# Kernel optimization log

Hardware: AMD Instinct MI355X
Metric: run time of the kernel (lower is better)

Reference implementation:

```python
import jax, jax.numpy as jnp
import numpy as np

B, S, D, V = 4, 1024, 512, 8192
SCALES = [1, 2, 4, 8, 16]   # nn.Parameter init; used via int(scale.item()) -> static
WIN = 8                     # min(8, S//2) in compute_semantic_coherence
EPS = 1e-5


def layer_norm(x, g, b):
    m = x.mean(-1, keepdims=True)
    v = ((x - m) ** 2).mean(-1, keepdims=True)
    return (x - m) / jnp.sqrt(v + EPS) * g + b


def setup_inputs() -> dict:
    key = jax.random.key(0)
    ks = jax.random.split(key, 24)
    n = lambda k, shape, s=0.02: (jax.random.normal(k, shape, jnp.float32) * s)
    return {
        "embeddings": jax.random.normal(ks[0], (B, S, D), jnp.float32),
        "token_ids": jax.random.randint(ks[1], (B, S), 0, V),
        "context_mask": jnp.ones((B, S), jnp.float32),
        "token_similarity": n(ks[2], (V, V)),
        "W_scale": n(ks[3], (len(SCALES), D), 0.05), "b_scale": jnp.zeros((D,), jnp.float32),
        "W_sem": n(ks[4], (1, D), 0.05), "b_sem": jnp.zeros((D,), jnp.float32),
        "W_ctx": n(ks[5], (D, D), 0.02), "b_ctx": jnp.zeros((D,), jnp.float32),
        "W_fuse": n(ks[6], (4 * D, D), 0.02), "b_fuse": jnp.zeros((D,), jnp.float32),
        "ln1_g": jnp.ones((D,), jnp.float32), "ln1_b": jnp.zeros((D,), jnp.float32),
        "ln2_g": jnp.ones((D,), jnp.float32), "ln2_b": jnp.zeros((D,), jnp.float32),
        "ln3_g": jnp.ones((D,), jnp.float32), "ln3_b": jnp.zeros((D,), jnp.float32),
        "W_e0": n(ks[7], (D, D), 0.02), "b_e0": jnp.zeros((D,), jnp.float32),
        "W_e1": n(ks[8], (D, D), 0.02), "b_e1": jnp.zeros((D,), jnp.float32),
        "W_e2": n(ks[9], (D, D), 0.02), "b_e2": jnp.zeros((D,), jnp.float32),
    }


def _forward(embeddings, token_ids, context_mask, token_similarity,
             W_scale, b_scale, W_sem, b_sem, W_ctx, b_ctx, W_fuse, b_fuse,
             ln1_g, ln1_b, ln2_g, ln2_b, ln3_g, ln3_b,
             W_e0, b_e0, W_e1, b_e1, W_e2, b_e2):
    phases = jnp.tanh(embeddings)  # [B,S,D]

    # --- multi-scale coherence via cumulative sums + cos angle-difference identity ---
    # mean_t cos(p_t - m) = cos(m)*mean(cos p) + sin(m)*mean(sin p) over each window
    z = jnp.zeros((B, 1, D), phases.dtype)
    cum_p = jnp.concatenate([z, jnp.cumsum(phases, 1)], 1)            # [B,S+1,D]
    cum_c = jnp.concatenate([z, jnp.cumsum(jnp.cos(phases), 1)], 1)
    cum_s = jnp.concatenate([z, jnp.cumsum(jnp.sin(phases), 1)], 1)
    cols = []
    for s in SCALES:
        wm = (cum_p[:, s:] - cum_p[:, :-s]) / s   # window mean  [B,S-s+1,D]
        ac = (cum_c[:, s:] - cum_c[:, :-s]) / s   # window mean cos
        asn = (cum_s[:, s:] - cum_s[:, :-s]) / s  # window mean sin
        coh = jnp.mean(jnp.cos(wm) * ac + jnp.sin(wm) * asn, -1)      # [B,S-s+1]
        cols.append(jnp.pad(coh, ((0, 0), (0, s - 1))))               # torch leaves tail zeros
    msc = jnp.stack(cols, -1)                                         # [B,S,num_scales]
    scale_coh = msc @ W_scale + b_scale                               # [B,S,D]

    # --- semantic coherence (windowed, sim-weighted; torch takes mean over WHOLE tensor incl. batch) ---
    te = token_similarity[token_ids]                                  # [B,S,V]
    ten = te / jnp.maximum(jnp.linalg.norm(te, axis=-1, keepdims=True), 1e-12)
    tsim = jnp.einsum('biv,bjv->bij', ten, ten)                       # [B,S,S]
    off = jnp.arange(-WIN, WIN + 1)
    pos = jnp.arange(S)[:, None] + off[None, :]                       # [S,17]
    valid = (pos >= 0) & (pos < S)
    posc = jnp.clip(pos, 0, S - 1)
    pwin = phases[:, posc]                                            # [B,S,17,D]
    swin = jnp.take_along_axis(tsim, jnp.broadcast_to(posc[None], (B, S, 2 * WIN + 1)), axis=2)
    coh = jnp.cos((phases[:, :, None, :] - pwin) * swin[..., None]) * valid[None, :, :, None].astype(phases.dtype)
    counts = valid.sum(1).astype(phases.dtype)                        # [S]
    sem = coh.sum((0, 2, 3)) / (B * counts * D)                       # [S] (same scalar for all batches)
    sem = jnp.broadcast_to(sem[None, :], (B, S))[..., None]           # [B,S,1]
    sem_coh = sem @ W_sem + b_sem                                     # [B,S,D]

    # --- context coherence (context_mask path) ---
    cmean = jnp.mean(embeddings * context_mask[..., None], 1, keepdims=True)
    ctx_coh = jnp.cos(embeddings - cmean) @ W_ctx + b_ctx

    # --- local coherence ---
    lc = jnp.cos(embeddings[:, 1:] - embeddings[:, :-1])
    lc = jnp.concatenate([lc, jnp.zeros((B, 1, D), embeddings.dtype)], 1)

    allc = jnp.concatenate([scale_coh, sem_coh, ctx_coh, lc], -1)     # [B,S,4D]
    x = layer_norm(allc @ W_fuse + b_fuse, ln1_g, ln1_b)
    x = jax.nn.gelu(x, approximate=False)                             # dropout = identity (eval)
    for W, bb in ((W_e0, b_e0), (W_e1, b_e1), (W_e2, b_e2)):
        r = x
        h = layer_norm(x, ln2_g, ln2_b) @ W + bb
        x = r + jax.nn.gelu(h, approximate=False) * 0.1
    return layer_norm(x, ln3_g, ln3_b)


def reference(embeddings, token_ids, context_mask, token_similarity,
              W_scale, b_scale, W_sem, b_sem, W_ctx, b_ctx, W_fuse, b_fuse,
              ln1_g, ln1_b, ln2_g, ln2_b, ln3_g, ln3_b,
              W_e0, b_e0, W_e1, b_e1, W_e2, b_e2):
    return _forward(embeddings, token_ids, context_mask, token_similarity,
                    W_scale, b_scale, W_sem, b_sem, W_ctx, b_ctx, W_fuse, b_fuse,
                    ln1_g, ln1_b, ln2_g, ln2_b, ln3_g, ln3_b,
                    W_e0, b_e0, W_e1, b_e1, W_e2, b_e2)
```

## Files before the change

kernel.cpp:

```cpp
#include <hip/hip_runtime.h>


#define DEV __device__ __forceinline__
typedef unsigned short u16;
typedef __bf16 bf16x8 __attribute__((ext_vector_type(8)));
typedef float f32x4 __attribute__((ext_vector_type(4)));

static constexpr int S = 1024;
static constexpr int D = 512;
static constexpr int KCAT = 1056;

DEV u16 f2bf(float f) {
  unsigned u = __float_as_uint(f);
  return (u16)((u + 0x7fffu + ((u >> 16) & 1u)) >> 16);
}
DEV float gelu(float x) { return 0.5f * x * (1.f + erff(x * 0.70710678118654752f)); }
DEV float wred(float v) {
#pragma unroll
  for (int off = 32; off; off >>= 1) v += __shfl_down(v, off, 64);
  return v;
}
DEV void bred2(float& a, float& b, float* sm, int tid) {
  a = wred(a); b = wred(b);
  int w = tid >> 6;
  if ((tid & 63) == 0) { sm[w] = a; sm[w + 4] = b; }
  __syncthreads();
  a = sm[0] + sm[1] + sm[2] + sm[3];
  b = sm[4] + sm[5] + sm[6] + sm[7];
  __syncthreads();
}

__global__ __launch_bounds__(256) void k_pre(const float* __restrict__ emb,
                                             const float* __restrict__ mask,
                                             float* __restrict__ ph,
                                             float* __restrict__ cmacc) {
  int blk = blockIdx.x, tid = threadIdx.x;
  if (blk < 1024) {
    int idx = blk * 256 + tid;
#pragma unroll
    for (int r = 0; r < 2; ++r, idx += 262144) {
      float4 v = ((const float4*)emb)[idx];
      float4 o;
      o.x = tanhf(v.x); o.y = tanhf(v.y); o.z = tanhf(v.z); o.w = tanhf(v.w);
      ((float4*)ph)[idx] = o;
    }
  } else {
    int r = blk - 1024, b = r >> 3, chunk = r & 7;
    float a0 = 0.f, a1 = 0.f;
    for (int s = chunk * 128; s < chunk * 128 + 128; ++s) {
      float m = mask[b * S + s];
      const float* row = emb + (size_t)(b * S + s) * D;
      a0 += row[tid] * m; a1 += row[tid + 256] * m;
    }
    atomicAdd(cmacc + b * D + tid, a0);
    atomicAdd(cmacc + b * D + tid + 256, a1);
  }
}

static constexpr int DP = 77;
__global__ __launch_bounds__(256) void k_dots(const float* __restrict__ sim,
                                              const int* __restrict__ tok,
                                              float* __restrict__ dots_raw,
                                              float* __restrict__ normsq) {
  __shared__ float sT[256 * DP];
  __shared__ int stok[72];
  int bx = blockIdx.x, cy = blockIdx.y, tid = threadIdx.x;
  int b = bx >> 4, g0 = (bx & 15) * 64;
  int gidx = b * S + g0;
  if (tid < 72) {
    int p = g0 + tid;
    stok[tid] = (p < S) ? tok[b * S + p] : -1;
  }
  __syncthreads();
  int c = tid, cbase = cy * 256;
#pragma unroll 3
  for (int it = 0; it < 18; ++it) {
#pragma unroll
    for (int j = 0; j < 4; ++j) {
      int tk = stok[it * 4 + j];
      sT[c * DP + it * 4 + j] = (tk >= 0) ? sim[(size_t)tk * 8192 + cbase + c] : 0.f;
    }
  }
  __syncthreads();
  int wave = tid >> 6, lane = tid & 63;
  float acc[9] = {};
#pragma unroll 2
  for (int cc = 0; cc < 64; ++cc) {
    const float* row = &sT[(wave * 64 + cc) * DP];
    float va = row[lane];
    acc[8] += va * va;
#pragma unroll
    for (int o = 1; o <= 8; ++o) acc[o - 1] += va * row[lane + o];
  }
  __syncthreads();
  float* red = sT;
#pragma unroll
  for (int s = 0; s < 9; ++s) red[(wave * 9 + s) * 64 + lane] = acc[s];
  __syncthreads();
  for (int u = tid; u < 576; u += 256) {
    int s = u >> 6, a = u & 63;
    float v = red[s * 64 + a] + red[(9 + s) * 64 + a] +
              red[(18 + s) * 64 + a] + red[(27 + s) * 64 + a];
    if (s < 8) atomicAdd(&dots_raw[(size_t)(gidx + a) * 8 + s], v);
    else       atomicAdd(&normsq[gidx + a], v);
  }
}

__global__ __launch_bounds__(256) void k_coh(const float* __restrict__ ph,
                                             const float* __restrict__ dots_raw,
                                             const float* __restrict__ normsq,
                                             float* __restrict__ msc,
                                             float* __restrict__ semacc) {
  __shared__ float sw[4][17];
  int wave = threadIdx.x >> 6, lane = threadIdx.x & 63;
  int idx = blockIdx.x * 4 + wave, i = idx & 1023;
  if (lane < 17) {
    int o = lane - 8, j = i + o;
    float v = 0.f;
    if (j >= 0 && j < S) {
      if (o == 0) v = 1.f;
      else {
        float dr = (o > 0) ? dots_raw[(size_t)idx * 8 + o - 1]
                           : dots_raw[(size_t)(idx + o) * 8 + (-o - 1)];
        float ni = fmaxf(sqrtf(normsq[idx]), 1e-12f);
        float nj = fmaxf(sqrtf(normsq[idx + o]), 1e-12f);
        v = dr / (ni * nj);
      }
    }
    sw[wave][lane] = v;
  }
  __syncthreads();
  int jmax = (S - 1 - i < 15) ? (S - 1 - i) : 15;
  float a0 = 0.f, a1 = 0.f, a2 = 0.f, a3 = 0.f, a4 = 0.f, asem = 0.f;
  for (int it = 0; it < 8; ++it) {
    int d = lane + it * 64;
    float p[24];
#pragma unroll
    for (int t = 0; t < 24; ++t) {
      int o = t - 8, j = i + o;
      int oc = (j >= 0 && j < S) ? o : 0;
      p[t] = ph[(size_t)(idx + oc) * D + d];
    }
    float sp = 0.f, sc = 0.f, ss = 0.f;
#pragma unroll
    for (int j = 0; j < 16; ++j) {
      float x = (j <= jmax) ? p[j + 8] : 0.f;
      sp += x; sc += __cosf(x); ss += __sinf(x);
      if (j == 0) a0 += __cosf(sp) * sc + __sinf(sp) * ss;
      else if (j == 1)  { float wm = sp * 0.5f;    a1 += __cosf(wm) * (sc * 0.5f)    + __sinf(wm) * (ss * 0.5f); }
      else if (j == 3)  { float wm = sp * 0.25f;   a2 += __cosf(wm) * (sc * 0.25f)   + __sinf(wm) * (ss * 0.25f); }
      else if (j == 7)  { float wm = sp * 0.125f;  a3 += __cosf(wm) * (sc * 0.125f)  + __sinf(wm) * (ss * 0.125f); }
      else if (j == 15) { float wm = sp * 0.0625f; a4 += __cosf(wm) * (sc * 0.0625f) + __sinf(wm) * (ss * 0.0625f); }
    }
    float p0 = p[8];
#pragma unroll
    for (int oi = 0; oi < 17; ++oi) {
      int o = oi - 8, j = i + o;
      bool valid = (j >= 0) && (j < S);
      float sv = sw[wave][oi];
      asem += valid ? __cosf((p0 - p[oi]) * sv) : 0.f;
    }
  }
  a0 = wred(a0); a1 = wred(a1); a2 = wred(a2); a3 = wred(a3); a4 = wred(a4);
  asem = wred(asem);
  if (lane == 0) {
    float* o = msc + (size_t)idx * 5;
    o[0] = a0 * (1.f / 512.f);
    o[1] = (jmax >= 1)  ? a1 * (1.f / 512.f) : 0.f;
    o[2] = (jmax >= 3)  ? a2 * (1.f / 512.f) : 0.f;
    o[3] = (jmax >= 7)  ? a3 * (1.f / 512.f) : 0.f;
    o[4] = (jmax >= 15) ? a4 * (1.f / 512.f) : 0.f;
    atomicAdd(semacc + i, asem);
  }
}

__global__ __launch_bounds__(256) void k_wbig(const float* __restrict__ W0,
    const float* __restrict__ W1, const float* __restrict__ W2,
    const float* __restrict__ Wf, const float* __restrict__ wctx,
    const float* __restrict__ Wsc, const float* __restrict__ Wsm,
    const float* __restrict__ bsc, const float* __restrict__ bsm,
    const float* __restrict__ bcx,
    u16* __restrict__ T0, u16* __restrict__ T1, u16* __restrict__ T2,
    u16* __restrict__ wcatT, float* __restrict__ ctx_acc,
    float* __restrict__ sm_acc) {
  __shared__ float tile[64][65];
  int blk = blockIdx.x, tid = threadIdx.x;
  if (blk < 256) {
    int z = blk >> 6, rem = blk & 63;
    const float* src = z == 0 ? W0 : z == 1 ? W1 : z == 2 ? W2 : Wf + (size_t)1536 * 512;
    int r0 = (rem >> 3) * 64, c0 = (rem & 7) * 64;
    int tr = tid >> 6, tc = tid & 63;
#pragma unroll 4
    for (int i = 0; i < 16; ++i)
      tile[tr + i * 4][tc] = src[(size_t)(r0 + tr + i * 4) * 512 + c0 + tc];
    __syncthreads();
#pragma unroll 4
    for (int i = 0; i < 16; ++i) {
      int n = c0 + tr + i * 4, k = r0 + tc;
      u16 v = f2bf(tile[tc][tr + i * 4]);
      if (z == 3) wcatT[(size_t)n * KCAT + 512 + k] = v;
      else (z == 0 ? T0 : z == 1 ? T1 : T2)[(size_t)n * 512 + k] = v;
    }
  } else if (blk < 512) {
    int rem = blk - 256;
    int n = (rem & 1) * 256 + tid;
    int kbase = ((rem & 63) >> 1) * 16;
    int j0 = (rem >> 6) * 128;
    float acc[16] = {};
    for (int j = j0; j < j0 + 128; ++j) {
      float wf3 = Wf[(size_t)(1024 + j) * 512 + n];
#pragma unroll
      for (int kk = 0; kk < 16; ++kk) acc[kk] += wctx[(size_t)(kbase + kk) * 512 + j] * wf3;
    }
#pragma unroll
    for (int kk = 0; kk < 16; ++kk)
      atomicAdd(&ctx_acc[(size_t)(kbase + kk) * 512 + n], acc[kk]);
  } else {
    int rem = blk - 512;
    int n = (rem & 1) * 256 + tid;
    int j0 = (rem >> 1) * 16;
    float a0 = 0.f, a1 = 0.f, a2 = 0.f, a3 = 0.f, a4 = 0.f, au = 0.f, ac = 0.f;
    for (int j = j0; j < j0 + 16; ++j) {
      float wf1 = Wf[(size_t)j * 512 + n];
      float wf2 = Wf[(size_t)(512 + j) * 512 + n];
      float wf3 = Wf[(size_t)(1024 + j) * 512 + n];
      a0 += Wsc[j] * wf1; a1 += Wsc[512 + j] * wf1; a2 += Wsc[1024 + j] * wf1;
      a3 += Wsc[1536 + j] * wf1; a4 += Wsc[2048 + j] * wf1;
      au += Wsm[j] * wf2;
      ac += bsc[j] * wf1 + bsm[j] * wf2 + bcx[j] * wf3;
    }
    atomicAdd(&sm_acc[0 * 512 + n], a0);
    atomicAdd(&sm_acc[1 * 512 + n], a1);
    atomicAdd(&sm_acc[2 * 512 + n], a2);
    atomicAdd(&sm_acc[3 * 512 + n], a3);
    atomicAdd(&sm_acc[4 * 512 + n], a4);
    atomicAdd(&sm_acc[5 * 512 + n], au);
    atomicAdd(&sm_acc[6 * 512 + n], ac);
  }
}

__global__ __launch_bounds__(256) void k_packfin(const float* __restrict__ ctx_acc,
    const float* __restrict__ sm_acc, const float* __restrict__ bfu,
    u16* __restrict__ wcatT) {
  __shared__ float tile[64][65];
  int blk = blockIdx.x, tid = threadIdx.x;
  if (blk < 64) {
    int r0 = (blk >> 3) * 64, c0 = (blk & 7) * 64;
    int tr = tid >> 6, tc = tid & 63;
#pragma unroll 4
    for (int i = 0; i < 16; ++i)
      tile[tr + i * 4][tc] = ctx_acc[(size_t)(r0 + tr + i * 4) * 512 + c0 + tc];
    __syncthreads();
#pragma unroll 4
    for (int i = 0; i < 16; ++i)
      wcatT[(size_t)(c0 + tr + i * 4) * KCAT + r0 + tc] = f2bf(tile[tc][tr + i * 4]);
  } else {
    int n = (blk - 64) * 256 + tid;
    u16* row = wcatT + (size_t)n * KCAT;
#pragma unroll
    for (int s = 0; s < 6; ++s) row[1024 + s] = f2bf(sm_acc[s * 512 + n]);
    row[1030] = f2bf(sm_acc[6 * 512 + n] + bfu[n]);
    for (int k = 1031; k < KCAT; ++k) row[k] = 0;
  }
}

__global__ __launch_bounds__(256) void k_xcat(const float* __restrict__ emb,
    const float* __restrict__ cmacc, const float* __restrict__ msc,
    const float* __restrict__ semacc, u16* __restrict__ xcat) {
  int idx = blockIdx.x, b = idx >> 10, i = idx & 1023, tid = threadIdx.x;
  const float* erow = emb + (size_t)idx * D;
  u16* orow = xcat + (size_t)idx * KCAT;
  for (int c = tid; c < KCAT; c += 256) {
    float v;
    if (c < 512) {
      v = __cosf(erow[c] - cmacc[b * D + c] * (1.f / 1024.f));
    } else if (c < 1024) {
      int d = c - 512;
      v = (i < S - 1) ? __cosf(erow[D + d] - erow[d]) : 0.f;
    } else if (c < 1029) {
      v = msc[(size_t)idx * 5 + (c - 1024)];
    } else if (c == 1029) {
      int cnt = ((i < 8) ? i : 8) + ((S - 1 - i < 8) ? (S - 1 - i) : 8) + 1;
      v = semacc[i] / (4.f * (float)cnt * 512.f);
    } else if (c == 1030) {
      v = 1.f;
    } else v = 0.f;
    orow[c] = f2bf(v);
  }
}

__global__ __launch_bounds__(256) void k_gemm(const u16* __restrict__ A,
    const u16* __restrict__ BT, float* __restrict__ C,
    const float* __restrict__ bias, int K) {
  __shared__ __align__(16) u16 sA[64 * 40];
  __shared__ __align__(16) u16 sB[64 * 40];
  int tid = threadIdx.x, wave = tid >> 6, lane = tid & 63;
  int m0 = blockIdx.x * 64, n0 = blockIdx.y * 64;
  int lr = tid >> 2, lc = (tid & 3) * 8;
  int q8 = (lane >> 4) * 8, l15 = lane & 15;
  const u16* Ap = A + (size_t)(m0 + lr) * K + lc;
  const u16* Bp = BT + (size_t)(n0 + lr) * K + lc;
  f32x4 acc[4] = {};
  for (int k0 = 0; k0 < K; k0 += 32) {
    *(uint4*)&sA[lr * 40 + lc] = *(const uint4*)(Ap + k0);
    *(uint4*)&sB[lr * 40 + lc] = *(const uint4*)(Bp + k0);
    __syncthreads();
    bf16x8 af = *(const bf16x8*)&sA[(wave * 16 + l15) * 40 + q8];
#pragma unroll
    for (int f = 0; f < 4; ++f) {
      bf16x8 bfr = *(const bf16x8*)&sB[(f * 16 + l15) * 40 + q8];
      acc[f] = __builtin_amdgcn_mfma_f32_16x16x32_bf16(af, bfr, acc[f], 0, 0, 0);
    }
    __syncthreads();
  }
  int r0 = m0 + wave * 16 + (lane >> 4) * 4;
#pragma unroll
  for (int f = 0; f < 4; ++f) {
    int col = n0 + f * 16 + l15;
    float bv = bias ? bias[col] : 0.f;
#pragma unroll
    for (int r = 0; r < 4; ++r)
      C[(size_t)(r0 + r) * 512 + col] = acc[f][r] + bv;
  }
}

__global__ __launch_bounds__(256) void k_post_y1(const float* __restrict__ y,
    float* __restrict__ x, u16* __restrict__ t,
    const float* __restrict__ g1, const float* __restrict__ b1,
    const float* __restrict__ g2, const float* __restrict__ b2) {
  __shared__ float sm[8];
  int row = blockIdx.x, tid = threadIdx.x;
  size_t base = (size_t)row * 512;
  float v0 = y[base + tid], v1 = y[base + tid + 256];
  float s = v0 + v1, ss = v0 * v0 + v1 * v1;
  bred2(s, ss, sm, tid);
  float m = s * (1.f / 512.f);
  float inv = rsqrtf(ss * (1.f / 512.f) - m * m + 1e-5f);
  float x0 = gelu((v0 - m) * inv * g1[tid] + b1[tid]);
  float x1 = gelu((v1 - m) * inv * g1[tid + 256] + b1[tid + 256]);
  x[base + tid] = x0; x[base + tid + 256] = x1;
  s = x0 + x1; ss = x0 * x0 + x1 * x1;
  bred2(s, ss, sm, tid);
  m = s * (1.f / 512.f);
  inv = rsqrtf(ss * (1.f / 512.f) - m * m + 1e-5f);
  t[base + tid] = f2bf((x0 - m) * inv * g2[tid] + b2[tid]);
  t[base + tid + 256] = f2bf((x1 - m) * inv * g2[tid + 256] + b2[tid + 256]);
}

__global__ __launch_bounds__(256) void k_post_res(const float* __restrict__ h,
    float* __restrict__ x, u16* __restrict__ t, float* __restrict__ out,
    const float* __restrict__ g, const float* __restrict__ bb, int final_) {
  __shared__ float sm[8];
  int row = blockIdx.x, tid = threadIdx.x;
  size_t base = (size_t)row * 512;
  float x0 = x[base + tid] + 0.1f * gelu(h[base + tid]);
  float x1 = x[base + tid + 256] + 0.1f * gelu(h[base + tid + 256]);
  float s = x0 + x1, ss = x0 * x0 + x1 * x1;
  bred2(s, ss, sm, tid);
  float m = s * (1.f / 512.f);
  float inv = rsqrtf(ss * (1.f / 512.f) - m * m + 1e-5f);
  float n0 = (x0 - m) * inv * g[tid] + bb[tid];
  float n1 = (x1 - m) * inv * g[tid + 256] + bb[tid + 256];
  if (final_) {
    out[base + tid] = n0; out[base + tid + 256] = n1;
  } else {
    x[base + tid] = x0; x[base + tid + 256] = x1;
    t[base + tid] = f2bf(n0); t[base + tid + 256] = f2bf(n1);
  }
}

extern "C" void kernel_launch(void* const* d_in, const int* in_sizes, int n_in,
                              void* d_out, int out_size, void* d_ws, size_t ws_size,
                              hipStream_t stream) {
  const float* emb     = (const float*)d_in[0];
  const int*   tok     = (const int*)d_in[1];
  const float* mask    = (const float*)d_in[2];
  const float* sim     = (const float*)d_in[3];
  const float* W_scale = (const float*)d_in[4];
  const float* b_scale = (const float*)d_in[5];
  const float* W_sem   = (const float*)d_in[6];
  const float* b_sem   = (const float*)d_in[7];
  const float* W_ctx   = (const float*)d_in[8];
  const float* b_ctx   = (const float*)d_in[9];
  const float* W_fuse  = (const float*)d_in[10];
  const float* b_fuse  = (const float*)d_in[11];
  const float* ln1_g = (const float*)d_in[12], *ln1_b = (const float*)d_in[13];
  const float* ln2_g = (const float*)d_in[14], *ln2_b = (const float*)d_in[15];
  const float* ln3_g = (const float*)d_in[16], *ln3_b = (const float*)d_in[17];
  const float* W_e0 = (const float*)d_in[18], *b_e0 = (const float*)d_in[19];
  const float* W_e1 = (const float*)d_in[20], *b_e1 = (const float*)d_in[21];
  const float* W_e2 = (const float*)d_in[22], *b_e2 = (const float*)d_in[23];
  float* out = (float*)d_out;

  char* w = (char*)d_ws; size_t off = 0;
  auto alloc = [&](size_t bytes) { void* p = w + off; off += (bytes + 255) & ~(size_t)255; return p; };
  float* phases = (float*)alloc((size_t)4096 * 512 * 4);
  float* hbuf   = (float*)alloc((size_t)4096 * 512 * 4);
  float* xbuf   = (float*)alloc((size_t)4096 * 512 * 4);
  u16*   tbuf   = (u16*)  alloc((size_t)4096 * 512 * 2);
  u16*   xcat   = (u16*)  alloc((size_t)4096 * KCAT * 2);
  u16*   wcatT  = (u16*)  alloc((size_t)512 * KCAT * 2);
  u16*   We0T   = (u16*)  alloc((size_t)512 * 512 * 2);
  u16*   We1T   = (u16*)  alloc((size_t)512 * 512 * 2);
  u16*   We2T   = (u16*)  alloc((size_t)512 * 512 * 2);
  float* msc    = (float*)alloc((size_t)4096 * 5 * 4);
  float* semacc   = (float*)alloc((size_t)1024 * 4);
  float* cmacc    = (float*)alloc((size_t)4 * 512 * 4);
  float* dots_raw = (float*)alloc((size_t)4096 * 8 * 4);
  float* normsq   = (float*)alloc((size_t)4096 * 4);
  float* ctx_acc  = (float*)alloc((size_t)512 * 512 * 4);
  float* sm_acc   = (float*)alloc((size_t)7 * 512 * 4);
  (void)ws_size; (void)in_sizes; (void)n_in; (void)out_size;

  size_t zbytes = (size_t)(1024 + 4 * 512 + 4096 * 8 + 4096 + 512 * 512 + 7 * 512) * 4;
  hipMemsetAsync(semacc, 0, zbytes, stream);

  k_pre<<<1056, 256, 0, stream>>>(emb, mask, phases, cmacc);
  k_dots<<<dim3(64, 32), 256, 0, stream>>>(sim, tok, dots_raw, normsq);
  k_coh<<<1024, 256, 0, stream>>>(phases, dots_raw, normsq, msc, semacc);

  k_wbig<<<576, 256, 0, stream>>>(W_e0, W_e1, W_e2, W_fuse, W_ctx,
                                  W_scale, W_sem, b_scale, b_sem, b_ctx,
                                  We0T, We1T, We2T, wcatT, ctx_acc, sm_acc);
  k_packfin<<<66, 256, 0, stream>>>(ctx_acc, sm_acc, b_fuse, wcatT);

  k_xcat<<<4096, 256, 0, stream>>>(emb, cmacc, msc, semacc, xcat);
  k_gemm<<<dim3(64, 8), 256, 0, stream>>>(xcat, wcatT, hbuf, nullptr, KCAT);
  k_post_y1<<<4096, 256, 0, stream>>>(hbuf, xbuf, tbuf, ln1_g, ln1_b, ln2_g, ln2_b);

  k_gemm<<<dim3(64, 8), 256, 0, stream>>>(tbuf, We0T, hbuf, b_e0, 512);
  k_post_res<<<4096, 256, 0, stream>>>(hbuf, xbuf, tbuf, nullptr, ln2_g, ln2_b, 0);
  k_gemm<<<dim3(64, 8), 256, 0, stream>>>(tbuf, We1T, hbuf, b_e1, 512);
  k_post_res<<<4096, 256, 0, stream>>>(hbuf, xbuf, tbuf, nullptr, ln2_g, ln2_b, 0);
  k_gemm<<<dim3(64, 8), 256, 0, stream>>>(tbuf, We2T, hbuf, b_e2, 512);
  k_post_res<<<4096, 256, 0, stream>>>(hbuf, xbuf, nullptr, out, ln3_g, ln3_b, 1);
}
```

Before: 656.0 us.

## Tile k_dots and k_coh through shared memory with coalesced float4 loads

k_dots now loads similarity rows as coalesced float4 into a 72x129 shared tile of 128 columns per block, with the grid doubled in y to cover all columns. k_coh is restructured from one wave per token (each lane reloading 24 neighbor rows from global) into blocks that stage an 88-row phase window in shared memory and split D into four slices. Partial sums are combined with atomics into a zeroed msc_raw buffer, and the window-validity masks and scaling move into k_xcat. This cuts redundant global reads of phases and the strided gathers, at the cost of more atomics and a larger memset.

```diff
diff --git a/kernel.cpp b/kernel.cpp
--- a/kernel.cpp
+++ b/kernel.cpp
@@ -28,6 +28,11 @@
   a = sm[0] + sm[1] + sm[2] + sm[3];
   b = sm[4] + sm[5] + sm[6] + sm[7];
   __syncthreads();
+}
+DEV float qred(float v) {
+  v += __shfl_xor(v, 1, 64);
+  v += __shfl_xor(v, 2, 64);
+  return v;
 }
 
 __global__ __launch_bounds__(256) void k_pre(const float* __restrict__ emb,
@@ -57,40 +62,40 @@
   }
 }
 
-static constexpr int DP = 77;
+static constexpr int CP = 129;
 __global__ __launch_bounds__(256) void k_dots(const float* __restrict__ sim,
                                               const int* __restrict__ tok,
                                               float* __restrict__ dots_raw,
                                               float* __restrict__ normsq) {
-  __shared__ float sT[256 * DP];
+  __shared__ float sT[72 * CP];
   __shared__ int stok[72];
   int bx = blockIdx.x, cy = blockIdx.y, tid = threadIdx.x;
-  int b = bx >> 4, g0 = (bx & 15) * 64;
-  int gidx = b * S + g0;
+  int b = bx >> 4, g0 = (bx & 15) * 64, gidx = b * S + g0;
   if (tid < 72) {
     int p = g0 + tid;
     stok[tid] = (p < S) ? tok[b * S + p] : -1;
   }
   __syncthreads();
-  int c = tid, cbase = cy * 256;
-#pragma unroll 3
-  for (int it = 0; it < 18; ++it) {
-#pragma unroll
-    for (int j = 0; j < 4; ++j) {
-      int tk = stok[it * 4 + j];
-      sT[c * DP + it * 4 + j] = (tk >= 0) ? sim[(size_t)tk * 8192 + cbase + c] : 0.f;
-    }
+  const float4* sim4 = (const float4*)sim;
+#pragma unroll
+  for (int it = 0; it < 9; ++it) {
+    int u = it * 256 + tid, r = u >> 5, q = u & 31;
+    int tk = stok[r];
+    float4 v = make_float4(0.f, 0.f, 0.f, 0.f);
+    if (tk >= 0) v = sim4[(size_t)tk * 2048 + cy * 32 + q];
+    float* dst = &sT[r * CP + 4 * q];
+    dst[0] = v.x; dst[1] = v.y; dst[2] = v.z; dst[3] = v.w;
   }
   __syncthreads();
   int wave = tid >> 6, lane = tid & 63;
   float acc[9] = {};
-#pragma unroll 2
-  for (int cc = 0; cc < 64; ++cc) {
-    const float* row = &sT[(wave * 64 + cc) * DP];
-    float va = row[lane];
+  const float* base = &sT[lane * CP + wave * 32];
+#pragma unroll 4
+  for (int cc = 0; cc < 32; ++cc) {
+    float va = base[cc];
     acc[8] += va * va;
 #pragma unroll
-    for (int o = 1; o <= 8; ++o) acc[o - 1] += va * row[lane + o];
+    for (int o = 1; o <= 8; ++o) acc[o - 1] += va * base[o * CP + cc];
   }
   __syncthreads();
   float* red = sT;
@@ -106,16 +111,29 @@
   }
 }
 
+static constexpr int CP2 = 132;
 __global__ __launch_bounds__(256) void k_coh(const float* __restrict__ ph,
                                              const float* __restrict__ dots_raw,
                                              const float* __restrict__ normsq,
-                                             float* __restrict__ msc,
+                                             float* __restrict__ msc_raw,
                                              float* __restrict__ semacc) {
-  __shared__ float sw[4][17];
-  int wave = threadIdx.x >> 6, lane = threadIdx.x & 63;
-  int idx = blockIdx.x * 4 + wave, i = idx & 1023;
-  if (lane < 17) {
-    int o = lane - 8, j = i + o;
+  __shared__ float sP[88 * CP2];
+  __shared__ float sw2[64 * 17];
+  int bx = blockIdx.x, dy = blockIdx.y, tid = threadIdx.x;
+  int b = bx >> 4, g0 = (bx & 15) * 64;
+  const float4* ph4 = (const float4*)ph;
+#pragma unroll
+  for (int it = 0; it < 11; ++it) {
+    int u = it * 256 + tid, r = u >> 5, q = u & 31;
+    int gr = g0 - 8 + r;
+    gr = gr < 0 ? 0 : (gr > S - 1 ? S - 1 : gr);
+    float4 v = ph4[(size_t)(b * S + gr) * 128 + dy * 32 + q];
+    *(float4*)&sP[r * CP2 + 4 * q] = v;
+  }
+  for (int u = tid; u < 1088; u += 256) {
+    int a = u / 17, oi = u - a * 17;
+    int i = g0 + a, o = oi - 8, j = i + o;
+    int idx = b * S + i;
     float v = 0.f;
     if (j >= 0 && j < S) {
       if (o == 0) v = 1.f;
@@ -127,24 +145,24 @@
         v = dr / (ni * nj);
       }
     }
-    sw[wave][lane] = v;
-  }
-  __syncthreads();
-  int jmax = (S - 1 - i < 15) ? (S - 1 - i) : 15;
+    sw2[u] = v;
+  }
+  __syncthreads();
+  int ar = tid >> 2, dq = tid & 3;
+  int i = g0 + ar, idx = b * S + i;
+  int jmax = S - 1 - i; if (jmax > 15) jmax = 15;
+  float swr[17];
+#pragma unroll
+  for (int oi = 0; oi < 17; ++oi) swr[oi] = sw2[ar * 17 + oi];
   float a0 = 0.f, a1 = 0.f, a2 = 0.f, a3 = 0.f, a4 = 0.f, asem = 0.f;
-  for (int it = 0; it < 8; ++it) {
-    int d = lane + it * 64;
-    float p[24];
-#pragma unroll
-    for (int t = 0; t < 24; ++t) {
-      int o = t - 8, j = i + o;
-      int oc = (j >= 0 && j < S) ? o : 0;
-      p[t] = ph[(size_t)(idx + oc) * D + d];
-    }
+#pragma unroll 2
+  for (int dd = 0; dd < 32; ++dd) {
+    int d = dq + 4 * dd;
+    const float* pb = &sP[(ar + 8) * CP2 + d];
     float sp = 0.f, sc = 0.f, ss = 0.f;
 #pragma unroll
     for (int j = 0; j < 16; ++j) {
-      float x = (j <= jmax) ? p[j + 8] : 0.f;
+      float x = (j <= jmax) ? pb[j * CP2] : 0.f;
       sp += x; sc += __cosf(x); ss += __sinf(x);
       if (j == 0) a0 += __cosf(sp) * sc + __sinf(sp) * ss;
       else if (j == 1)  { float wm = sp * 0.5f;    a1 += __cosf(wm) * (sc * 0.5f)    + __sinf(wm) * (ss * 0.5f); }
@@ -152,24 +170,22 @@
       else if (j == 7)  { float wm = sp * 0.125f;  a3 += __cosf(wm) * (sc * 0.125f)  + __sinf(wm) * (ss * 0.125f); }
       else if (j == 15) { float wm = sp * 0.0625f; a4 += __cosf(wm) * (sc * 0.0625f) + __sinf(wm) * (ss * 0.0625f); }
     }
-    float p0 = p[8];
+    float p0 = pb[0];
+    const float* qb = &sP[ar * CP2 + d];
 #pragma unroll
     for (int oi = 0; oi < 17; ++oi) {
-      int o = oi - 8, j = i + o;
+      int j = i + oi - 8;
       bool valid = (j >= 0) && (j < S);
-      float sv = sw[wave][oi];
-      asem += valid ? __cosf((p0 - p[oi]) * sv) : 0.f;
-    }
-  }
-  a0 = wred(a0); a1 = wred(a1); a2 = wred(a2); a3 = wred(a3); a4 = wred(a4);
-  asem = wred(asem);
-  if (lane == 0) {
-    float* o = msc + (size_t)idx * 5;
-    o[0] = a0 * (1.f / 512.f);
-    o[1] = (jmax >= 1)  ? a1 * (1.f / 512.f) : 0.f;
-    o[2] = (jmax >= 3)  ? a2 * (1.f / 512.f) : 0.f;
-    o[3] = (jmax >= 7)  ? a3 * (1.f / 512.f) : 0.f;
-    o[4] = (jmax >= 15) ? a4 * (1.f / 512.f) : 0.f;
+      float pj = qb[oi * CP2];
+      asem += valid ? __cosf((p0 - pj) * swr[oi]) : 0.f;
+    }
+  }
+  a0 = qred(a0); a1 = qred(a1); a2 = qred(a2); a3 = qred(a3); a4 = qred(a4);
+  asem = qred(asem);
+  if (dq == 0) {
+    float* mr = msc_raw + (size_t)idx * 5;
+    atomicAdd(mr + 0, a0); atomicAdd(mr + 1, a1); atomicAdd(mr + 2, a2);
+    atomicAdd(mr + 3, a3); atomicAdd(mr + 4, a4);
     atomicAdd(semacc + i, asem);
   }
 }
@@ -265,7 +281,7 @@
 }
 
 __global__ __launch_bounds__(256) void k_xcat(const float* __restrict__ emb,
-    const float* __restrict__ cmacc, const float* __restrict__ msc,
+    const float* __restrict__ cmacc, const float* __restrict__ msc_raw,
     const float* __restrict__ semacc, u16* __restrict__ xcat) {
   int idx = blockIdx.x, b = idx >> 10, i = idx & 1023, tid = threadIdx.x;
   const float* erow = emb + (size_t)idx * D;
@@ -278,7 +294,8 @@
       int d = c - 512;
       v = (i < S - 1) ? __cosf(erow[D + d] - erow[d]) : 0.f;
     } else if (c < 1029) {
-      v = msc[(size_t)idx * 5 + (c - 1024)];
+      int s = c - 1024, req = (1 << s) - 1;
+      v = (S - 1 - i >= req) ? msc_raw[(size_t)idx * 5 + s] * (1.f / 512.f) : 0.f;
     } else if (c == 1029) {
       int cnt = ((i < 8) ? i : 8) + ((S - 1 - i < 8) ? (S - 1 - i) : 8) + 1;
       v = semacc[i] / (4.f * (float)cnt * 512.f);
@@ -403,28 +420,28 @@
   u16*   We0T   = (u16*)  alloc((size_t)512 * 512 * 2);
   u16*   We1T   = (u16*)  alloc((size_t)512 * 512 * 2);
   u16*   We2T   = (u16*)  alloc((size_t)512 * 512 * 2);
-  float* msc    = (float*)alloc((size_t)4096 * 5 * 4);
   float* semacc   = (float*)alloc((size_t)1024 * 4);
   float* cmacc    = (float*)alloc((size_t)4 * 512 * 4);
   float* dots_raw = (float*)alloc((size_t)4096 * 8 * 4);
   float* normsq   = (float*)alloc((size_t)4096 * 4);
+  float* msc_raw  = (float*)alloc((size_t)4096 * 5 * 4);
   float* ctx_acc  = (float*)alloc((size_t)512 * 512 * 4);
   float* sm_acc   = (float*)alloc((size_t)7 * 512 * 4);
   (void)ws_size; (void)in_sizes; (void)n_in; (void)out_size;
 
-  size_t zbytes = (size_t)(1024 + 4 * 512 + 4096 * 8 + 4096 + 512 * 512 + 7 * 512) * 4;
+  size_t zbytes = (size_t)(1024 + 4 * 512 + 4096 * 8 + 4096 + 4096 * 5 + 512 * 512 + 7 * 512) * 4;
   hipMemsetAsync(semacc, 0, zbytes, stream);
 
   k_pre<<<1056, 256, 0, stream>>>(emb, mask, phases, cmacc);
-  k_dots<<<dim3(64, 32), 256, 0, stream>>>(sim, tok, dots_raw, normsq);
-  k_coh<<<1024, 256, 0, stream>>>(phases, dots_raw, normsq, msc, semacc);
+  k_dots<<<dim3(64, 64), 256, 0, stream>>>(sim, tok, dots_raw, normsq);
+  k_coh<<<dim3(64, 4), 256, 0, stream>>>(phases, dots_raw, normsq, msc_raw, semacc);
 
   k_wbig<<<576, 256, 0, stream>>>(W_e0, W_e1, W_e2, W_fuse, W_ctx,
                                   W_scale, W_sem, b_scale, b_sem, b_ctx,
                                   We0T, We1T, We2T, wcatT, ctx_acc, sm_acc);
   k_packfin<<<66, 256, 0, stream>>>(ctx_acc, sm_acc, b_fuse, wcatT);
 
-  k_xcat<<<4096, 256, 0, stream>>>(emb, cmacc, msc, semacc, xcat);
+  k_xcat<<<4096, 256, 0, stream>>>(emb, cmacc, msc_raw, semacc, xcat);
   k_gemm<<<dim3(64, 8), 256, 0, stream>>>(xcat, wcatT, hbuf, nullptr, KCAT);
   k_post_y1<<<4096, 256, 0, stream>>>(hbuf, xbuf, tbuf, ln1_g, ln1_b, ln2_g, ln2_b);
 
```

Result: faster. 609.6 us (-7.1%).
